# Kernel optimization log

Hardware: AMD Instinct MI355X
Metric: run time of the kernel (lower is better)

The kernel has to match this reference:

```python
import jax, jax.numpy as jnp
import numpy as np

V, B, C, H, W, D, G = 5, 1, 32, 384, 384, 4, 8


def _rot(a, b, c):
    ca, sa = np.cos(a), np.sin(a)
    cb, sb = np.cos(b), np.sin(b)
    cc, sc = np.cos(c), np.sin(c)
    Rx = np.array([[1, 0, 0], [0, ca, -sa], [0, sa, ca]])
    Ry = np.array([[cb, 0, sb], [0, 1, 0], [-sb, 0, cb]])
    Rz = np.array([[cc, -sc, 0], [sc, cc, 0], [0, 0, 1]])
    return (Rz @ Ry @ Rx).astype(np.float32)


def setup_inputs():
    key = jax.random.key(0)
    ks = jax.random.split(key, 8)
    features = jax.random.normal(ks[0], (V, B, C, H, W), jnp.float32)
    current_depths = jax.random.uniform(ks[1], (B, D, H, W), jnp.float32, 425.0, 935.0)
    rng = np.random.RandomState(0)
    Ks = np.zeros((B, V, 3, 3), np.float32)
    Es = np.zeros((B, V, 3, 4), np.float32)
    for b in range(B):
        for v in range(V):
            f = 0.8 * W * (1.0 + 0.01 * rng.randn())
            Ks[b, v] = np.array([[f, 0, W / 2.0], [0, f, H / 2.0], [0, 0, 1.0]], np.float32)
            if v == 0:
                Rm = np.eye(3, dtype=np.float32)
                t = np.zeros(3, np.float32)
            else:
                Rm = _rot(*(0.02 * rng.randn(3)))
                t = np.array([25.0 * v, 5.0 * rng.randn(), 5.0 * rng.randn()], np.float32)
            Es[b, v, :, :3] = Rm
            Es[b, v, :, 3] = t
    w0 = 0.3 * jax.random.normal(ks[2], (16, G), jnp.float32)
    b0 = jnp.zeros((16,), jnp.float32)
    w1 = 0.3 * jax.random.normal(ks[3], (8, 16), jnp.float32)
    b1 = jnp.zeros((8,), jnp.float32)
    w2 = 0.3 * jax.random.normal(ks[4], (1, 8), jnp.float32)
    b2 = jnp.zeros((1,), jnp.float32)
    return {"features": features, "current_depths": current_depths,
            "cam_intrinsic": jnp.asarray(Ks), "cam_extrinsic": jnp.asarray(Es),
            "w0": w0, "b0": b0, "w1": w1, "b1": b1, "w2": w2, "b2": b2}


def _bilinear_sample(feat, px, py):
    # feat [B,C,H,W]; px,py [B,N] pixel coords (align_corners=True), zero padding
    Bn, Cn, Hn, Wn = feat.shape
    ff = feat.reshape(Bn, Cn, Hn * Wn)
    x0 = jnp.floor(px)
    y0 = jnp.floor(py)
    wx1 = px - x0
    wx0 = 1.0 - wx1
    wy1 = py - y0
    wy0 = 1.0 - wy1

    def gather(xi, yi, w):
        valid = (xi >= 0) & (xi <= Wn - 1) & (yi >= 0) & (yi <= Hn - 1)
        xc = jnp.clip(xi, 0, Wn - 1).astype(jnp.int32)
        yc = jnp.clip(yi, 0, Hn - 1).astype(jnp.int32)
        idx = yc * Wn + xc  # [B,N]
        v = jnp.take_along_axis(ff, idx[:, None, :], axis=2)  # [B,C,N]
        return v * (w * valid)[:, None, :]

    return (gather(x0, y0, wx0 * wy0) + gather(x0 + 1.0, y0, wx1 * wy0)
            + gather(x0, y0 + 1.0, wx0 * wy1) + gather(x0 + 1.0, y0 + 1.0, wx1 * wy1))


def _pixelwise_net(sim, w0, b0, w1, b1, w2, b2):
    # PixelwiseNet: 1x1x1 Conv3d G->16->8->1 (BN folded to identity, eval stats), sigmoid, max over depth
    x = jax.nn.relu(jnp.einsum('og,bgdhw->bodhw', w0, sim) + b0[None, :, None, None, None])
    x = jax.nn.relu(jnp.einsum('oc,bcdhw->bodhw', w1, x) + b1[None, :, None, None, None])
    x = jnp.einsum('oc,bcdhw->bodhw', w2, x) + b2[None, :, None, None, None]
    return jnp.max(jax.nn.sigmoid(x), axis=2)  # [B,1,H,W]


def reference(features, current_depths, cam_intrinsic, cam_extrinsic, w0, b0, w1, b1, w2, b2):
    ref_feat = features[0]                                   # [B,C,H,W]
    ref_g = ref_feat.reshape(B, G, C // G, H, W)
    # pixel grid with half-pixel centers, homogeneous [3, H*W]
    xs = jnp.arange(W, dtype=jnp.float32) + 0.5
    ys = jnp.arange(H, dtype=jnp.float32) + 0.5
    gx, gy = jnp.meshgrid(xs, ys)                            # [H,W]
    grid = jnp.stack([gx.ravel(), gy.ravel(), jnp.ones(H * W, jnp.float32)], 0)
    K_ref_inv = jnp.linalg.inv(cam_intrinsic[:, 0])          # [B,3,3]
    R = cam_extrinsic[:, :, :3, :3]                          # [B,V,3,3]
    t = cam_extrinsic[:, :, :3, 3:4]                         # [B,V,3,1]
    R_ref_inv = jnp.linalg.inv(R[:, 0])                      # [B,3,3]
    uv = jnp.einsum('bij,jn->bin', K_ref_inv, grid)          # [B,3,HW]
    cam_pts = uv[:, None] * current_depths.reshape(B, D, 1, H * W)   # [B,D,3,HW]
    world = jnp.einsum('bij,bdjn->bdin', R_ref_inv, cam_pts - t[:, 0:1])
    world = world.transpose(0, 2, 1, 3).reshape(B, 3, D * H * W)     # [B,3,N], N=D*H*W
    sim_sum = 0.0
    w_sum = 0.0
    for s in range(1, V):
        cp = jnp.einsum('bij,bjn->bin', R[:, s], world) + t[:, s]    # [B,3,N]
        uvd = jnp.einsum('bij,bjn->bin', cam_intrinsic[:, s], cp)
        z = uvd[:, 2] + 1e-9
        px = uvd[:, 0] / z
        py = uvd[:, 1] / z
        warped = _bilinear_sample(features[s], px, py)               # [B,C,N]
        warped = warped.reshape(B, G, C // G, D, H, W)
        sim = jnp.mean(warped * ref_g[:, :, :, None], axis=2)        # [B,G,D,H,W]
        vw = _pixelwise_net(sim, w0, b0, w1, b1, w2, b2)             # [B,1,H,W]
        sim_sum = sim_sum + sim * vw[:, :, None]
        w_sum = w_sum + vw[:, :, None]
    return sim_sum / w_sum
```

## Files before the change

### kernel.cpp

```cpp
#include <hip/hip_runtime.h>
#include <math.h>

#define Vn 5
#define Cn 32
#define Hn 384
#define Wn 384
#define Dn 4
#define Gn 8
#define HWn (Hn*Wn)

typedef _Float16 h2 __attribute__((ext_vector_type(2)));

__device__ __forceinline__ float fdot2h(h2 a, h2 b, float c){
#if __has_builtin(__builtin_amdgcn_fdot2)
    return __builtin_amdgcn_fdot2(a, b, c, false);
#else
    return (float)a.x*(float)b.x + (float)a.y*(float)b.y + c;
#endif
}
__device__ __forceinline__ unsigned int packh2(float a, float b){
    h2 h;
    h.x = (_Float16)a;
    h.y = (_Float16)b;
    return __builtin_bit_cast(unsigned int, h);
}

__device__ __forceinline__ void inv3(const float* m, float* o){
    float a=m[0],b=m[1],c=m[2],d=m[3],e=m[4],f=m[5],g=m[6],h=m[7],i=m[8];
    float A =  e*i - f*h;
    float B = -(d*i - f*g);
    float C =  d*h - e*g;
    float det = a*A + b*B + c*C;
    float r = 1.f/det;
    o[0] = A*r;            o[1] = -(b*i - c*h)*r;  o[2] =  (b*f - c*e)*r;
    o[3] = B*r;            o[4] =  (a*i - c*g)*r;  o[5] = -(a*f - c*d)*r;
    o[6] = C*r;            o[7] = -(a*h - b*g)*r;  o[8] =  (a*e - b*d)*r;
}
__device__ __forceinline__ void mm3(const float* a, const float* b, float* o){
    #pragma unroll
    for (int r=0;r<3;r++)
        #pragma unroll
        for (int c=0;c<3;c++)
            o[r*3+c] = a[r*3+0]*b[0*3+c] + a[r*3+1]*b[1*3+c] + a[r*3+2]*b[2*3+c];
}
__device__ __forceinline__ void mv3(const float* a, const float* v, float* o){
    #pragma unroll
    for (int r=0;r<3;r++)
        o[r] = a[r*3+0]*v[0] + a[r*3+1]*v[1] + a[r*3+2]*v[2];
}

__global__ __launch_bounds__(256)
void transpose_kernel(const float* __restrict__ feat, unsigned short* __restrict__ featT){
    const int s  = blockIdx.y;
    const int p0 = blockIdx.x * 1024 + threadIdx.x * 4;
    const float* src = feat + (size_t)(s+1)*Cn*HWn + p0;
    unsigned int outw[4][16];
    #pragma unroll
    for (int c=0; c<Cn; c+=2){
        const float4 a = *(const float4*)(src + (size_t)c*HWn);
        const float4 b = *(const float4*)(src + (size_t)(c+1)*HWn);
        outw[0][c>>1] = packh2(a.x, b.x);
        outw[1][c>>1] = packh2(a.y, b.y);
        outw[2][c>>1] = packh2(a.z, b.z);
        outw[3][c>>1] = packh2(a.w, b.w);
    }
    uint4* dst = (uint4*)(featT + ((size_t)s*HWn + p0)*Cn);
    #pragma unroll
    for (int p=0;p<4;p++){
        #pragma unroll
        for (int q=0;q<4;q++){
            uint4 o;
            o.x = outw[p][4*q+0];
            o.y = outw[p][4*q+1];
            o.z = outw[p][4*q+2];
            o.w = outw[p][4*q+3];
            dst[p*4+q] = o;
        }
    }
}

#define DOTG(uA, uB, g, WV)                                                    \
    {                                                                          \
        const h2 pa = __builtin_bit_cast(h2, (uA));                            \
        const h2 pb = __builtin_bit_cast(h2, (uB));                            \
        const float dt = fdot2h(pa, r2[2*(g)], fdot2h(pb, r2[2*(g)+1], 0.f));  \
        sg[(g)] = fmaf((WV), dt, sg[(g)]);                                     \
    }

#define TAPDOT(Q0, Q1, Q2, Q3, WT)                                             \
    DOTG((Q0).x, (Q0).y, 0, WT)                                                \
    DOTG((Q0).z, (Q0).w, 1, WT)                                                \
    DOTG((Q1).x, (Q1).y, 2, WT)                                                \
    DOTG((Q1).z, (Q1).w, 3, WT)                                                \
    DOTG((Q2).x, (Q2).y, 4, WT)                                                \
    DOTG((Q2).z, (Q2).w, 5, WT)                                                \
    DOTG((Q3).x, (Q3).y, 6, WT)                                                \
    DOTG((Q3).z, (Q3).w, 7, WT)

__global__ __launch_bounds__(256, 2)
void gbinet_kernel(const float* __restrict__ feat,
                   const float* __restrict__ depths,
                   const float* __restrict__ Kin,
                   const float* __restrict__ Ein,
                   const float* __restrict__ w0, const float* __restrict__ b0,
                   const float* __restrict__ w1, const float* __restrict__ b1,
                   const float* __restrict__ w2, const float* __restrict__ b2,
                   const unsigned short* __restrict__ featT,
                   float* __restrict__ out)
{
    __shared__ float sW0[128], sW1[128], sB0[16], sB1[8], sW2[8], sB2s[1];
    __shared__ float sM[48];
    __shared__ float sRef[64*33];
    __shared__ float sDep[4*65];
    __shared__ float sOut[64*33];
    const int t = threadIdx.x;
    if (t < 128){ sW0[t] = w0[t]; sW1[t] = w1[t]; }
    if (t < 16) sB0[t] = b0[t];
    if (t < 8){ sB1[t] = b1[t]; sW2[t] = w2[t]; }

    const int bid = blockIdx.x;
    const int sid = (bid & 7) * (HWn/64/8) + (bid >> 3);
    const int blockBase = sid * 64;

    {
        const float* srcR = feat + blockBase;
        #pragma unroll
        for (int k=0;k<8;k++){
            const int i  = k*256 + t;
            const int c  = i >> 6;
            const int px = i & 63;
            sRef[px*33 + c] = srcR[(size_t)c*HWn + px];
        }
        const int dp = t >> 6;
        const int px = t & 63;
        sDep[dp*65 + px] = depths[(size_t)dp*HWn + blockBase + px];
    }

    if (t == 0){
        sB2s[0] = b2[0];
        float K0inv[9]; inv3(Kin, K0inv);
        float R0[9], t0[3];
        #pragma unroll
        for (int r=0;r<3;r++){
            #pragma unroll
            for (int c=0;c<3;c++) R0[r*3+c] = Ein[r*4+c];
            t0[r] = Ein[r*4+3];
        }
        float R0inv[9]; inv3(R0, R0inv);
        float M0[9]; mm3(R0inv, K0inv, M0);
        float Rt0[3]; mv3(R0inv, t0, Rt0);
        for (int s=1;s<Vn;s++){
            const float* Ks = Kin + s*9;
            const float* Es = Ein + s*12;
            float Rs[9], ts[3];
            #pragma unroll
            for (int r=0;r<3;r++){
                #pragma unroll
                for (int c=0;c<3;c++) Rs[r*3+c] = Es[r*4+c];
                ts[r] = Es[r*4+3];
            }
            float T1[9]; mm3(Rs, M0, T1);
            float A[9];  mm3(Ks, T1, A);
            float Rr[3]; mv3(Rs, Rt0, Rr);
            float tv[3] = { ts[0]-Rr[0], ts[1]-Rr[1], ts[2]-Rr[2] };
            float cv[3]; mv3(Ks, tv, cv);
            float* dm = &sM[(s-1)*12];
            #pragma unroll
            for (int i=0;i<9;i++) dm[i] = A[i];
            #pragma unroll
            for (int i=0;i<3;i++) dm[9+i] = cv[i];
        }
    }
    __syncthreads();

    const int pixLocal = t >> 2;
    const int s        = t & 3;
    const int pix      = blockBase + pixLocal;
    const float xg = (float)(pix % Wn) + 0.5f;
    const float yg = (float)(pix / Wn) + 0.5f;

    h2 r2[16];
    #pragma unroll
    for (int k=0;k<16;k++){
        r2[k].x = (_Float16)sRef[pixLocal*33 + 2*k];
        r2[k].y = (_Float16)sRef[pixLocal*33 + 2*k+1];
    }
    float dep[Dn];
    #pragma unroll
    for (int d=0;d<Dn;d++) dep[d] = sDep[d*65 + pixLocal];

    const float* M = &sM[s*12];
    const float bx = M[0]*xg + M[1]*yg + M[2];
    const float by = M[3]*xg + M[4]*yg + M[5];
    const float bz = M[6]*xg + M[7]*yg + M[8];
    const float cx = M[9], cy = M[10], cz = M[11];
    const unsigned short* vbase = featT + (size_t)s*HWn*Cn;

    float sim[Gn][Dn];
    #pragma unroll
    for (int d=0;d<Dn;d++){
        const float dd = dep[d];
        const float ux = fmaf(bx, dd, cx);
        const float uy = fmaf(by, dd, cy);
        const float uz = fmaf(bz, dd, cz) + 1e-9f;
        const float rz = 1.f/uz;
        const float px = ux*rz, py = uy*rz;
        const float x0 = floorf(px), y0 = floorf(py);
        const float wx1 = px - x0, wy1 = py - y0;
        const float wx0 = 1.f - wx1, wy0 = 1.f - wy1;
        const bool vx0 = (x0 >= 0.f)     && (x0 <= (float)(Wn-1));
        const bool vx1 = (x0 >= -1.f)    && (x0 <= (float)(Wn-2));
        const bool vy0 = (y0 >= 0.f)     && (y0 <= (float)(Hn-1));
        const bool vy1 = (y0 >= -1.f)    && (y0 <= (float)(Hn-2));
        const float w00 = (vx0&&vy0) ? 0.25f*wx0*wy0 : 0.f;
        const float w10 = (vx1&&vy0) ? 0.25f*wx1*wy0 : 0.f;
        const float w01 = (vx0&&vy1) ? 0.25f*wx0*wy1 : 0.f;
        const float w11 = (vx1&&vy1) ? 0.25f*wx1*wy1 : 0.f;
        const int xi0 = (int)fminf(fmaxf(x0,     0.f), (float)(Wn-1));
        const int xi1 = (int)fminf(fmaxf(x0+1.f, 0.f), (float)(Wn-1));
        const int yi0 = (int)fminf(fmaxf(y0,     0.f), (float)(Hn-1));
        const int yi1 = (int)fminf(fmaxf(y0+1.f, 0.f), (float)(Hn-1));

        const uint4* pA = (const uint4*)(vbase + ((size_t)yi0*Wn + xi0)*Cn);
        const uint4* pB = (const uint4*)(vbase + ((size_t)yi0*Wn + xi1)*Cn);
        const uint4* pC = (const uint4*)(vbase + ((size_t)yi1*Wn + xi0)*Cn);
        const uint4* pD = (const uint4*)(vbase + ((size_t)yi1*Wn + xi1)*Cn);
        const uint4 A0 = pA[0], A1 = pA[1], A2 = pA[2], A3 = pA[3];
        const uint4 B0 = pB[0], B1 = pB[1], B2 = pB[2], B3 = pB[3];
        const uint4 C0 = pC[0], C1 = pC[1], C2 = pC[2], C3 = pC[3];
        const uint4 D0 = pD[0], D1 = pD[1], D2 = pD[2], D3 = pD[3];

        float sg[Gn];
        #pragma unroll
        for (int g=0; g<Gn; g++) sg[g] = 0.f;
        TAPDOT(A0, A1, A2, A3, w00)
        TAPDOT(B0, B1, B2, B3, w10)
        TAPDOT(C0, C1, C2, C3, w01)
        TAPDOT(D0, D1, D2, D3, w11)
        #pragma unroll
        for (int g=0; g<Gn; g++) sim[g][d] = sg[g];
    }

    float maxlog = -3.0e38f;
    #pragma unroll
    for (int dp=0; dp<2; dp++){
        const int d0 = 2*dp, d1 = 2*dp+1;
        float hx[16], hy[16];
        #pragma unroll
        for (int o=0;o<16;o++){
            float ax = sB0[o], ay = sB0[o];
            #pragma unroll
            for (int g=0; g<Gn; g++){
                const float wv = sW0[o*Gn+g];
                ax = fmaf(wv, sim[g][d0], ax);
                ay = fmaf(wv, sim[g][d1], ay);
            }
            hx[o] = fmaxf(ax, 0.f);
            hy[o] = fmaxf(ay, 0.f);
        }
        float lgx = sB2s[0], lgy = sB2s[0];
        #pragma unroll
        for (int o=0;o<8;o++){
            float ax = sB1[o], ay = sB1[o];
            #pragma unroll
            for (int i=0;i<16;i++){
                const float wv = sW1[o*16+i];
                ax = fmaf(wv, hx[i], ax);
                ay = fmaf(wv, hy[i], ay);
            }
            const float w2v = sW2[o];
            lgx = fmaf(w2v, fmaxf(ax, 0.f), lgx);
            lgy = fmaf(w2v, fmaxf(ay, 0.f), lgy);
        }
        maxlog = fmaxf(maxlog, fmaxf(lgx, lgy));
    }
    const float vw = 1.f/(1.f + __expf(-maxlog));

    float wsum = vw;
    wsum += __shfl_xor(wsum, 1);
    wsum += __shfl_xor(wsum, 2);
    #pragma unroll
    for (int g=0;g<Gn;g++)
        #pragma unroll
        for (int d=0;d<Dn;d++){
            float v = sim[g][d]*vw;
            v += __shfl_xor(v, 1);
            v += __shfl_xor(v, 2);
            sim[g][d] = v;
        }

    if (s == 0){
        const float invw = 1.f/wsum;
        #pragma unroll
        for (int g=0;g<Gn;g++)
            #pragma unroll
            for (int d=0;d<Dn;d++)
                sOut[pixLocal*33 + g*Dn + d] = sim[g][d]*invw;
    }
    __syncthreads();

    float* oBase = out + blockBase;
    #pragma unroll
    for (int k=0;k<8;k++){
        const int e     = k*256 + t;
        const int plane = e >> 6;
        const int pixel = e & 63;
        oBase[(size_t)plane*HWn + pixel] = sOut[pixel*33 + plane];
    }
}

extern "C" void kernel_launch(void* const* d_in, const int* in_sizes, int n_in,
                              void* d_out, int out_size, void* d_ws, size_t ws_size,
                              hipStream_t stream)
{
    (void)in_sizes; (void)n_in; (void)out_size; (void)ws_size;
    const float* feat   = (const float*)d_in[0];
    const float* depths = (const float*)d_in[1];
    const float* K      = (const float*)d_in[2];
    const float* E      = (const float*)d_in[3];
    const float* w0     = (const float*)d_in[4];
    const float* b0     = (const float*)d_in[5];
    const float* w1     = (const float*)d_in[6];
    const float* b1     = (const float*)d_in[7];
    const float* w2     = (const float*)d_in[8];
    const float* b2     = (const float*)d_in[9];
    float* out = (float*)d_out;
    unsigned short* featT = (unsigned short*)d_ws;

    dim3 g(HWn/1024, Vn-1);
    transpose_kernel<<<g, 256, 0, stream>>>(feat, featT);
    gbinet_kernel<<<HWn/64, 256, 0, stream>>>(feat, depths, K, E,
                                              w0,b0,w1,b1,w2,b2, featT, out);
}
```

Before: 276.8 us.

## Skip zero-weight bilinear taps, pack MLP math into float2 FMA, parallelize matrix setup

The four bilinear corner gathers now sit behind a per-tap branch, so out-of-bounds taps with zero weight skip their 64-byte loads and dot products. The pixelwise MLP is rewritten with two-wide float vectors so the compiler can emit packed FP32 FMA/max instructions. The per-view projection matrices are now computed by four threads in parallel rather than serially by one thread. The cost is that the branch may cause wave divergence and delay issuing the loads, which reduces memory-level parallelism.

```diff
diff --git a/kernel.cpp b/kernel.cpp
--- a/kernel.cpp
+++ b/kernel.cpp
@@ -10,6 +10,7 @@
 #define HWn (Hn*Wn)
 
 typedef _Float16 h2 __attribute__((ext_vector_type(2)));
+typedef float    f2 __attribute__((ext_vector_type(2)));
 
 __device__ __forceinline__ float fdot2h(h2 a, h2 b, float c){
 #if __has_builtin(__builtin_amdgcn_fdot2)
@@ -24,6 +25,9 @@
     h.y = (_Float16)b;
     return __builtin_bit_cast(unsigned int, h);
 }
+__device__ __forceinline__ f2 fma2(f2 a, f2 b, f2 c){ return __builtin_elementwise_fma(a, b, c); }
+__device__ __forceinline__ f2 max2(f2 a, f2 b){ return __builtin_elementwise_max(a, b); }
+__device__ __forceinline__ f2 splat2(float x){ f2 r; r.x = x; r.y = x; return r; }
 
 __device__ __forceinline__ void inv3(const float* m, float* o){
     float a=m[0],b=m[1],c=m[2],d=m[3],e=m[4],f=m[5],g=m[6],h=m[7],i=m[8];
@@ -87,15 +91,26 @@
         sg[(g)] = fmaf((WV), dt, sg[(g)]);                                     \
     }
 
-#define TAPDOT(Q0, Q1, Q2, Q3, WT)                                             \
-    DOTG((Q0).x, (Q0).y, 0, WT)                                                \
-    DOTG((Q0).z, (Q0).w, 1, WT)                                                \
-    DOTG((Q1).x, (Q1).y, 2, WT)                                                \
-    DOTG((Q1).z, (Q1).w, 3, WT)                                                \
-    DOTG((Q2).x, (Q2).y, 4, WT)                                                \
-    DOTG((Q2).z, (Q2).w, 5, WT)                                                \
-    DOTG((Q3).x, (Q3).y, 6, WT)                                                \
-    DOTG((Q3).z, (Q3).w, 7, WT)
+__device__ __forceinline__ void tap_f16(const unsigned short* __restrict__ vbase,
+                                        int xc, int yc, float w,
+                                        const h2* r2, float* sg)
+{
+    if (w != 0.f){
+        const uint4* p = (const uint4*)(vbase + ((size_t)yc*Wn + xc)*Cn);
+        const uint4 q0 = p[0];
+        const uint4 q1 = p[1];
+        const uint4 q2 = p[2];
+        const uint4 q3 = p[3];
+        DOTG(q0.x, q0.y, 0, w)
+        DOTG(q0.z, q0.w, 1, w)
+        DOTG(q1.x, q1.y, 2, w)
+        DOTG(q1.z, q1.w, 3, w)
+        DOTG(q2.x, q2.y, 4, w)
+        DOTG(q2.z, q2.w, 5, w)
+        DOTG(q3.x, q3.y, 6, w)
+        DOTG(q3.z, q3.w, 7, w)
+    }
+}
 
 __global__ __launch_bounds__(256, 2)
 void gbinet_kernel(const float* __restrict__ feat,
@@ -136,8 +151,7 @@
         sDep[dp*65 + px] = depths[(size_t)dp*HWn + blockBase + px];
     }
 
-    if (t == 0){
-        sB2s[0] = b2[0];
+    if (t < 4){
         float K0inv[9]; inv3(Kin, K0inv);
         float R0[9], t0[3];
         #pragma unroll
@@ -149,28 +163,28 @@
         float R0inv[9]; inv3(R0, R0inv);
         float M0[9]; mm3(R0inv, K0inv, M0);
         float Rt0[3]; mv3(R0inv, t0, Rt0);
-        for (int s=1;s<Vn;s++){
-            const float* Ks = Kin + s*9;
-            const float* Es = Ein + s*12;
-            float Rs[9], ts[3];
-            #pragma unroll
-            for (int r=0;r<3;r++){
-                #pragma unroll
-                for (int c=0;c<3;c++) Rs[r*3+c] = Es[r*4+c];
-                ts[r] = Es[r*4+3];
-            }
-            float T1[9]; mm3(Rs, M0, T1);
-            float A[9];  mm3(Ks, T1, A);
-            float Rr[3]; mv3(Rs, Rt0, Rr);
-            float tv[3] = { ts[0]-Rr[0], ts[1]-Rr[1], ts[2]-Rr[2] };
-            float cv[3]; mv3(Ks, tv, cv);
-            float* dm = &sM[(s-1)*12];
-            #pragma unroll
-            for (int i=0;i<9;i++) dm[i] = A[i];
-            #pragma unroll
-            for (int i=0;i<3;i++) dm[9+i] = cv[i];
-        }
-    }
+        const int sv = t + 1;
+        const float* Ks = Kin + sv*9;
+        const float* Es = Ein + sv*12;
+        float Rs[9], ts[3];
+        #pragma unroll
+        for (int r=0;r<3;r++){
+            #pragma unroll
+            for (int c=0;c<3;c++) Rs[r*3+c] = Es[r*4+c];
+            ts[r] = Es[r*4+3];
+        }
+        float T1[9]; mm3(Rs, M0, T1);
+        float A[9];  mm3(Ks, T1, A);
+        float Rr[3]; mv3(Rs, Rt0, Rr);
+        float tv[3] = { ts[0]-Rr[0], ts[1]-Rr[1], ts[2]-Rr[2] };
+        float cv[3]; mv3(Ks, tv, cv);
+        float* dm = &sM[t*12];
+        #pragma unroll
+        for (int i=0;i<9;i++) dm[i] = A[i];
+        #pragma unroll
+        for (int i=0;i<3;i++) dm[9+i] = cv[i];
+    }
+    if (t == 4) sB2s[0] = b2[0];
     __syncthreads();
 
     const int pixLocal = t >> 2;
@@ -221,22 +235,13 @@
         const int yi0 = (int)fminf(fmaxf(y0,     0.f), (float)(Hn-1));
         const int yi1 = (int)fminf(fmaxf(y0+1.f, 0.f), (float)(Hn-1));
 
-        const uint4* pA = (const uint4*)(vbase + ((size_t)yi0*Wn + xi0)*Cn);
-        const uint4* pB = (const uint4*)(vbase + ((size_t)yi0*Wn + xi1)*Cn);
-        const uint4* pC = (const uint4*)(vbase + ((size_t)yi1*Wn + xi0)*Cn);
-        const uint4* pD = (const uint4*)(vbase + ((size_t)yi1*Wn + xi1)*Cn);
-        const uint4 A0 = pA[0], A1 = pA[1], A2 = pA[2], A3 = pA[3];
-        const uint4 B0 = pB[0], B1 = pB[1], B2 = pB[2], B3 = pB[3];
-        const uint4 C0 = pC[0], C1 = pC[1], C2 = pC[2], C3 = pC[3];
-        const uint4 D0 = pD[0], D1 = pD[1], D2 = pD[2], D3 = pD[3];
-
         float sg[Gn];
         #pragma unroll
         for (int g=0; g<Gn; g++) sg[g] = 0.f;
-        TAPDOT(A0, A1, A2, A3, w00)
-        TAPDOT(B0, B1, B2, B3, w10)
-        TAPDOT(C0, C1, C2, C3, w01)
-        TAPDOT(D0, D1, D2, D3, w11)
+        tap_f16(vbase, xi0, yi0, w00, r2, sg);
+        tap_f16(vbase, xi1, yi0, w10, r2, sg);
+        tap_f16(vbase, xi0, yi1, w01, r2, sg);
+        tap_f16(vbase, xi1, yi1, w11, r2, sg);
         #pragma unroll
         for (int g=0; g<Gn; g++) sim[g][d] = sg[g];
     }
@@ -245,34 +250,28 @@
     #pragma unroll
     for (int dp=0; dp<2; dp++){
         const int d0 = 2*dp, d1 = 2*dp+1;
-        float hx[16], hy[16];
+        f2 sv[Gn];
+        #pragma unroll
+        for (int g=0; g<Gn; g++){ sv[g].x = sim[g][d0]; sv[g].y = sim[g][d1]; }
+        f2 h[16];
         #pragma unroll
         for (int o=0;o<16;o++){
-            float ax = sB0[o], ay = sB0[o];
-            #pragma unroll
-            for (int g=0; g<Gn; g++){
-                const float wv = sW0[o*Gn+g];
-                ax = fmaf(wv, sim[g][d0], ax);
-                ay = fmaf(wv, sim[g][d1], ay);
-            }
-            hx[o] = fmaxf(ax, 0.f);
-            hy[o] = fmaxf(ay, 0.f);
-        }
-        float lgx = sB2s[0], lgy = sB2s[0];
+            f2 a = splat2(sB0[o]);
+            #pragma unroll
+            for (int g=0; g<Gn; g++)
+                a = fma2(splat2(sW0[o*Gn+g]), sv[g], a);
+            h[o] = max2(a, splat2(0.f));
+        }
+        f2 lg = splat2(sB2s[0]);
         #pragma unroll
         for (int o=0;o<8;o++){
-            float ax = sB1[o], ay = sB1[o];
-            #pragma unroll
-            for (int i=0;i<16;i++){
-                const float wv = sW1[o*16+i];
-                ax = fmaf(wv, hx[i], ax);
-                ay = fmaf(wv, hy[i], ay);
-            }
-            const float w2v = sW2[o];
-            lgx = fmaf(w2v, fmaxf(ax, 0.f), lgx);
-            lgy = fmaf(w2v, fmaxf(ay, 0.f), lgy);
-        }
-        maxlog = fmaxf(maxlog, fmaxf(lgx, lgy));
+            f2 a = splat2(sB1[o]);
+            #pragma unroll
+            for (int i=0;i<16;i++)
+                a = fma2(splat2(sW1[o*16+i]), h[i], a);
+            lg = fma2(splat2(sW2[o]), max2(a, splat2(0.f)), lg);
+        }
+        maxlog = fmaxf(maxlog, fmaxf(lg.x, lg.y));
     }
     const float vw = 1.f/(1.f + __expf(-maxlog));
 
```

Measured after the change: 244.1 us. -11.8%, faster.
